# Performance work log

Measured on AMD Instinct MI355X. Metric: run time of the kernel, lower is better.

## Reference

```python
import jax, jax.numpy as jnp
import numpy as np

N_NODES = 50000
D_FEAT = 128
N_EDGES = 1_600_000
NUM_ITERATIONS = 20  # init kwarg num_iterations


def setup_inputs() -> dict:
    key = jax.random.key(0)
    k1, k2, k3 = jax.random.split(key, 3)
    x = jax.random.normal(k1, (N_NODES, D_FEAT), dtype=jnp.float32)
    edge_index = jax.random.randint(k2, (2, N_EDGES), 0, N_NODES, dtype=jnp.int32)
    mask = jax.random.bernoulli(k3, 0.5, (N_NODES, D_FEAT))  # True where feature is known
    return {"x": x, "edge_index": edge_index, "mask": mask}


def reference(x, edge_index, mask):
    row, col = edge_index[0], edge_index[1]
    # D^-1/2 A D^-1/2 edge weights (degree computed over col, as in the torch code)
    deg = jax.ops.segment_sum(jnp.ones((N_EDGES,), x.dtype), col, num_segments=N_NODES)
    deg_inv_sqrt = jnp.where(deg > 0, jax.lax.rsqrt(deg), 0.0)
    w = deg_inv_sqrt[row] * deg_inv_sqrt[col]  # [n_edges]

    out0 = jnp.where(mask, x, 0.0)  # zero out unknown features

    def body(_, out):
        # SpMM: result[i] = sum over edges e with row[e]==i of w[e] * out[col[e]]
        msg = w[:, None] * out[col]  # [n_edges, d]
        out = jax.ops.segment_sum(msg, row, num_segments=N_NODES)
        return jnp.where(mask, x, out)  # reset known features each iteration

    return jax.lax.fori_loop(0, NUM_ITERATIONS, body, out0)
```

## Files before the change

kernel.cpp:

```cpp
#include <hip/hip_runtime.h>

#define N_NODES 50000
#define D_FEAT 128
#define N_EDGES 1600000
#define NUM_ITERS 20
#define ZERO_NODE N_NODES
#define HNB 128
#define HALF_NODES 25000
#define NB 196
#define BCAP 192
#define ABLK 128
#define PAD 4
#define STAGE_CAP 12544
#define CSR_MAX (N_EDGES + PAD * N_NODES)

typedef unsigned int u32;
typedef unsigned short u16;
typedef unsigned long long u64;

__device__ __forceinline__ u16 bf16_rne(float f) {
    u32 u = __float_as_uint(f);
    u32 r = u + 0x7fffu + ((u >> 16) & 1u);
    return (u16)(r >> 16);
}

__global__ void detect_kernel(const u32* __restrict__ w, int nwords,
                              u32* __restrict__ flags) {
    int i = blockIdx.x * blockDim.x + threadIdx.x;
    int stride = gridDim.x * blockDim.x;
    u32 f = 0;
    for (; i < nwords; i += stride) {
        u32 v = w[i];
        if (v > 1u) f |= 1u;
        if (v == 0x3f800000u) f |= 2u;
    }
    if (f) atomicOr(flags, f);
}

__global__ void __launch_bounds__(256) hist_kernel(const int* __restrict__ idx,
                                                   u32* __restrict__ partial, int n) {
    __shared__ u32 h[HALF_NODES / 2];
    for (int i = threadIdx.x; i < HALF_NODES / 2; i += 256) h[i] = 0;
    __syncthreads();
    const int half = blockIdx.x >> 7;
    const int bid = blockIdx.x & (HNB - 1);
    const int base_node = half * HALF_NODES;
    int i = bid * 256 + threadIdx.x;
    const int stride = HNB * 256;
    for (; i < n; i += stride) {
        u32 r = (u32)(idx[i] - base_node);
        if (r < (u32)HALF_NODES) atomicAdd(&h[r >> 1], 1u << ((r & 1) * 16));
    }
    __syncthreads();
    u32* dst = partial + (size_t)bid * (N_NODES / 2) + half * (HALF_NODES / 2);
    for (int j = threadIdx.x; j < HALF_NODES / 2; j += 256) dst[j] = h[j];
}

__global__ void reduce_dis_kernel(const u32* __restrict__ pA, float* __restrict__ dis) {
    int i = blockIdx.x * blockDim.x + threadIdx.x;
    if (i >= N_NODES / 2) return;
    u32 sa = 0;
    for (int b = 0; b < HNB; ++b) sa += pA[(size_t)b * (N_NODES / 2) + i];
    int d0 = (int)(sa & 0xffffu), d1 = (int)(sa >> 16);
    dis[2 * i]     = d0 ? rsqrtf((float)d0) : 0.0f;
    dis[2 * i + 1] = d1 ? rsqrtf((float)d1) : 0.0f;
}

__global__ void __launch_bounds__(256) bucketA_kernel(const int* __restrict__ row,
                                                      const int* __restrict__ col,
                                                      u32* __restrict__ bucket,
                                                      int* __restrict__ bcnt) {
    __shared__ u32 cur[NB];
    for (int i = threadIdx.x; i < NB; i += 256) cur[i] = 0;
    __syncthreads();
    u32* myreg = bucket + (size_t)blockIdx.x * NB * BCAP;
    int i = blockIdx.x * 256 + threadIdx.x;
    int stride = gridDim.x * 256;
    for (; i < N_EDGES; i += stride) {
        int r = row[i];
        int b = r >> 8;
        u32 pos = atomicAdd(&cur[b], 1u);
        if (pos < (u32)BCAP)
            myreg[(size_t)b * BCAP + pos] = ((u32)(r & 255) << 16) | (u32)col[i];
    }
    __syncthreads();
    for (int i2 = threadIdx.x; i2 < NB; i2 += 256)
        bcnt[blockIdx.x * NB + i2] = (int)min(cur[i2], (u32)BCAP);
}

__global__ void __launch_bounds__(256) b1_kernel(const u32* __restrict__ bucket,
                                                 const int* __restrict__ bcnt,
                                                 int* __restrict__ cnt_p) {
    const int b = blockIdx.x;
    const int tid = threadIdx.x;
    __shared__ int pfx[ABLK + 1];
    __shared__ int cnts[ABLK];
    __shared__ u32 hist[256];
    if (tid < 256) hist[tid] = 0;
    if (tid < ABLK) cnts[tid] = bcnt[tid * NB + b];
    __syncthreads();
    if (tid == 0) {
        int s = 0;
        for (int k = 0; k < ABLK; ++k) { pfx[k] = s; s += cnts[k]; }
        pfx[ABLK] = s;
    }
    __syncthreads();
    const int total = pfx[ABLK];
    for (int t = tid; t < total; t += 256) {
        int lo = 0, hi = ABLK;
        while (hi - lo > 1) { int mid = (lo + hi) >> 1; if (pfx[mid] <= t) lo = mid; else hi = mid; }
        u32 e = bucket[(size_t)lo * NB * BCAP + (size_t)b * BCAP + (t - pfx[lo])];
        atomicAdd(&hist[e >> 16], 1u);
    }
    __syncthreads();
    const int r0 = b << 8;
    if (tid < 256) {
        int r = r0 + tid;
        if (r < N_NODES) cnt_p[r] = ((int)hist[tid] + (PAD - 1)) & ~(PAD - 1);
    }
}

__global__ void __launch_bounds__(1024) scan_kernel(const int* __restrict__ cnt,
                                                    int* __restrict__ offsets, int n) {
    __shared__ int wsum[16];
    __shared__ int s_carry;
    const int tid = threadIdx.x;
    const int lane = tid & 63, wid = tid >> 6;
    if (tid == 0) s_carry = 0;
    __syncthreads();
    for (int base = 0; base < n; base += 4096) {
        int i4 = base + tid * 4;
        int4 v = make_int4(0, 0, 0, 0);
        if (i4 < n) v = *(const int4*)(cnt + i4);
        int e1 = v.x, e2 = v.x + v.y, e3 = e2 + v.z, tot = e3 + v.w;
        int winc = tot;
        #pragma unroll
        for (int off = 1; off < 64; off <<= 1) {
            int t = __shfl_up(winc, off);
            if (lane >= off) winc += t;
        }
        if (lane == 63) wsum[wid] = winc;
        __syncthreads();
        if (tid < 16) {
            int s = wsum[tid];
            #pragma unroll
            for (int off = 1; off < 16; off <<= 1) {
                int t = __shfl_up(s, off);
                if (tid >= off) s += t;
            }
            wsum[tid] = s;
        }
        __syncthreads();
        int bb = s_carry + (wid ? wsum[wid - 1] : 0) + winc - tot;
        if (i4 < n) *(int4*)(offsets + i4) = make_int4(bb, bb + e1, bb + e2, bb + e3);
        __syncthreads();
        if (tid == 0) s_carry += wsum[15];
        __syncthreads();
    }
    if (tid == 0) offsets[n] = s_carry;
}

__global__ void __launch_bounds__(256) b2_kernel(const u32* __restrict__ bucket,
                                                 const int* __restrict__ bcnt,
                                                 const int* __restrict__ offsets,
                                                 u16* __restrict__ csr) {
    const int b = blockIdx.x;
    const int tid = threadIdx.x;
    const int r0 = b << 8;
    const int rcount = min(256, N_NODES - r0);
    __shared__ int pfx[ABLK + 1];
    __shared__ int cnts[ABLK];
    __shared__ int lbase[257];
    __shared__ u32 lcur[256];
    __shared__ __align__(16) u16 stage[STAGE_CAP];
    if (tid < ABLK) cnts[tid] = bcnt[tid * NB + b];
    for (int j = tid; j <= rcount; j += 256) lbase[j] = offsets[r0 + j] - offsets[r0];
    if (tid < 256) lcur[tid] = 0;
    __syncthreads();
    if (tid == 0) {
        int s = 0;
        for (int k = 0; k < ABLK; ++k) { pfx[k] = s; s += cnts[k]; }
        pfx[ABLK] = s;
    }
    __syncthreads();
    const int total = pfx[ABLK];
    const int L = min(lbase[rcount], STAGE_CAP);
    for (int j = tid; j < L; j += 256) stage[j] = (u16)ZERO_NODE;
    __syncthreads();
    for (int t = tid; t < total; t += 256) {
        int lo = 0, hi = ABLK;
        while (hi - lo > 1) { int mid = (lo + hi) >> 1; if (pfx[mid] <= t) lo = mid; else hi = mid; }
        u32 e = bucket[(size_t)lo * NB * BCAP + (size_t)b * BCAP + (t - pfx[lo])];
        int lr = (int)(e >> 16);
        u32 p = atomicAdd(&lcur[lr], 1u);
        int idx = lbase[lr] + (int)p;
        if (idx < STAGE_CAP) stage[idx] = (u16)(e & 0xffffu);
    }
    __syncthreads();
    uint4* dst = (uint4*)(csr + offsets[r0]);
    const uint4* src = (const uint4*)stage;
    for (int j = tid; j < (L >> 3); j += 256) dst[j] = src[j];
    if (tid == 0 && (L & 7)) {
        uint2* d2 = (uint2*)(csr + offsets[r0] + (L & ~7));
        const uint2* s2 = (const uint2*)(stage + (L & ~7));
        *d2 = *s2;
    }
}

__global__ void build_kernel(const void* __restrict__ mask,
                             const u32* __restrict__ flags,
                             const float* __restrict__ x,
                             const float* __restrict__ dis,
                             u32* __restrict__ bits,
                             u16* __restrict__ sxm, int n) {
    int i = blockIdx.x * blockDim.x + threadIdx.x;
    if (i >= n) return;
    u32 fl = *flags;
    int mv;
    if ((fl & 1u) == 0u) {
        mv = ((const int*)mask)[i];
    } else if (fl & 2u) {
        mv = (((const float*)mask)[i] != 0.0f) ? 1 : 0;
    } else {
        mv = ((const unsigned char*)mask)[i];
    }
    bool pred = (mv != 0);
    u64 b = __ballot(pred);
    int lane = threadIdx.x & 63;
    if (lane == 0)  bits[i >> 5] = (u32)b;
    if (lane == 32) bits[i >> 5] = (u32)(b >> 32);
    sxm[i] = pred ? bf16_rne(dis[i >> 7] * x[i]) : (u16)0;
}

template <bool FINAL>
__global__ void __launch_bounds__(256) prop_kernel(const int* __restrict__ offsets,
                                                   const u16* __restrict__ csr,
                                                   const u16* __restrict__ cur,
                                                   const u32* __restrict__ bits,
                                                   const float* __restrict__ dis,
                                                   const u16* __restrict__ sxm,
                                                   const float* __restrict__ x,
                                                   void* __restrict__ nxtp) {
    const int tid = threadIdx.x;
    const int wid = tid >> 6, lane = tid & 63;
    const int node = blockIdx.x * 4 + wid;
    if (node >= N_NODES) return;
    const int fl = lane & 15, eg = lane >> 4;
    const int s = offsets[node], e = offsets[node + 1];

    float a0 = 0, a1 = 0, a2 = 0, a3 = 0, a4 = 0, a5 = 0, a6 = 0, a7 = 0;
    #pragma unroll 8
    for (int base = s; base < e; base += 4) {
        const int c = (int)csr[base + eg];
        const uint4 r = *((const uint4*)(cur + (size_t)c * D_FEAT) + fl);
        a0 += __uint_as_float(r.x << 16);
        a1 += __uint_as_float(r.x & 0xffff0000u);
        a2 += __uint_as_float(r.y << 16);
        a3 += __uint_as_float(r.y & 0xffff0000u);
        a4 += __uint_as_float(r.z << 16);
        a5 += __uint_as_float(r.z & 0xffff0000u);
        a6 += __uint_as_float(r.w << 16);
        a7 += __uint_as_float(r.w & 0xffff0000u);
    }
    a0 += __shfl_xor(a0, 16); a0 += __shfl_xor(a0, 32);
    a1 += __shfl_xor(a1, 16); a1 += __shfl_xor(a1, 32);
    a2 += __shfl_xor(a2, 16); a2 += __shfl_xor(a2, 32);
    a3 += __shfl_xor(a3, 16); a3 += __shfl_xor(a3, 32);
    a4 += __shfl_xor(a4, 16); a4 += __shfl_xor(a4, 32);
    a5 += __shfl_xor(a5, 16); a5 += __shfl_xor(a5, 32);
    a6 += __shfl_xor(a6, 16); a6 += __shfl_xor(a6, 32);
    a7 += __shfl_xor(a7, 16); a7 += __shfl_xor(a7, 32);

    if (eg == 0) {
        const int fbase = node * D_FEAT + fl * 8;
        const u32 mb = (bits[node * 4 + (fl >> 2)] >> ((fl & 3) * 8)) & 0xffu;
        const float dr = dis[node];
        if (FINAL) {
            const float4 x0 = *(const float4*)(x + fbase);
            const float4 x1 = *(const float4*)(x + fbase + 4);
            float* outp = (float*)nxtp;
            float4 o0, o1;
            o0.x = (mb & 0x01u) ? x0.x : dr * a0;
            o0.y = (mb & 0x02u) ? x0.y : dr * a1;
            o0.z = (mb & 0x04u) ? x0.z : dr * a2;
            o0.w = (mb & 0x08u) ? x0.w : dr * a3;
            o1.x = (mb & 0x10u) ? x1.x : dr * a4;
            o1.y = (mb & 0x20u) ? x1.y : dr * a5;
            o1.z = (mb & 0x40u) ? x1.z : dr * a6;
            o1.w = (mb & 0x80u) ? x1.w : dr * a7;
            *(float4*)(outp + fbase) = o0;
            *(float4*)(outp + fbase + 4) = o1;
        } else {
            const float d2 = dr * dr;
            const uint4 sv = *(const uint4*)(sxm + fbase);
            u16 t0 = (mb & 0x01u) ? (u16)(sv.x)       : bf16_rne(d2 * a0);
            u16 t1 = (mb & 0x02u) ? (u16)(sv.x >> 16) : bf16_rne(d2 * a1);
            u16 t2 = (mb & 0x04u) ? (u16)(sv.y)       : bf16_rne(d2 * a2);
            u16 t3 = (mb & 0x08u) ? (u16)(sv.y >> 16) : bf16_rne(d2 * a3);
            u16 t4 = (mb & 0x10u) ? (u16)(sv.z)       : bf16_rne(d2 * a4);
            u16 t5 = (mb & 0x20u) ? (u16)(sv.z >> 16) : bf16_rne(d2 * a5);
            u16 t6 = (mb & 0x40u) ? (u16)(sv.w)       : bf16_rne(d2 * a6);
            u16 t7 = (mb & 0x80u) ? (u16)(sv.w >> 16) : bf16_rne(d2 * a7);
            uint4 st;
            st.x = (u32)t0 | ((u32)t1 << 16);
            st.y = (u32)t2 | ((u32)t3 << 16);
            st.z = (u32)t4 | ((u32)t5 << 16);
            st.w = (u32)t6 | ((u32)t7 << 16);
            *(uint4*)(((u16*)nxtp) + fbase) = st;
        }
    }
}

extern "C" void kernel_launch(void* const* d_in, const int* in_sizes, int n_in,
                              void* d_out, int out_size, void* d_ws, size_t ws_size,
                              hipStream_t stream) {
    const float* x = (const float*)d_in[0];
    const int* edge = (const int*)d_in[1];
    const void* mask = d_in[2];
    const int* row = edge;
    const int* col = edge + N_EDGES;
    float* out = (float*)d_out;

    char* ws = (char*)d_ws;
    size_t off = 0;
    auto alloc = [&](size_t bytes) -> void* {
        void* p = ws + off;
        off += (bytes + 255) & ~(size_t)255;
        return p;
    };
    const size_t state_elems = (size_t)(N_NODES + 1) * D_FEAT;
    int*   offsets = (int*)alloc((size_t)(N_NODES + 1) * 4);
    int*   cnt_p   = (int*)alloc((size_t)N_NODES * 4);
    float* dis     = (float*)alloc((size_t)N_NODES * 4);
    u32*   flags   = (u32*)alloc(256);
    u32*   bits    = (u32*)alloc((size_t)N_NODES * D_FEAT / 8);
    u32*   pA      = (u32*)alloc((size_t)HNB * (N_NODES / 2) * 4);
    u32*   bucket  = (u32*)alloc((size_t)ABLK * NB * BCAP * 4);
    int*   bcnt    = (int*)alloc((size_t)ABLK * NB * 4);
    u16*   csr     = (u16*)alloc((size_t)CSR_MAX * 2);
    u16*   sxm     = (u16*)alloc(state_elems * 2);
    u16*   stA     = (u16*)alloc(state_elems * 2);
    u16*   stB     = (u16*)alloc(state_elems * 2);

    hipMemsetAsync(flags, 0, 4, stream);
    hipMemsetAsync(sxm + (size_t)N_NODES * D_FEAT, 0, D_FEAT * 2, stream);
    hipMemsetAsync(stA + (size_t)N_NODES * D_FEAT, 0, D_FEAT * 2, stream);
    hipMemsetAsync(stB + (size_t)N_NODES * D_FEAT, 0, D_FEAT * 2, stream);

    const int total_feat = N_NODES * D_FEAT;
    const int mask_words = total_feat / 4;

    detect_kernel<<<1024, 256, 0, stream>>>((const u32*)mask, mask_words, flags);
    hist_kernel<<<2 * HNB, 256, 0, stream>>>(col, pA, N_EDGES);
    reduce_dis_kernel<<<(N_NODES / 2 + 255) / 256, 256, 0, stream>>>(pA, dis);
    bucketA_kernel<<<ABLK, 256, 0, stream>>>(row, col, bucket, bcnt);
    b1_kernel<<<NB, 256, 0, stream>>>(bucket, bcnt, cnt_p);
    scan_kernel<<<1, 1024, 0, stream>>>(cnt_p, offsets, N_NODES);
    build_kernel<<<total_feat / 256, 256, 0, stream>>>(mask, flags, x, dis, bits, sxm, total_feat);
    b2_kernel<<<NB, 256, 0, stream>>>(bucket, bcnt, offsets, csr);

    const int prop_blocks = (N_NODES + 3) / 4;
    const u16* src = sxm;
    for (int it = 0; it < NUM_ITERS; ++it) {
        if (it < NUM_ITERS - 1) {
            u16* dst = (it & 1) ? stB : stA;
            prop_kernel<false><<<prop_blocks, 256, 0, stream>>>(offsets, csr, src, bits, dis, sxm, x, dst);
            src = dst;
        } else {
            prop_kernel<true><<<prop_blocks, 256, 0, stream>>>(offsets, csr, src, bits, dis, sxm, x, out);
        }
    }
}
```

Baseline: 1.146 ms.

## Slice feature state into 16-wide column panels and stage CSR chunks in LDS

```diff
diff --git a/kernel.cpp b/kernel.cpp
--- a/kernel.cpp
+++ b/kernel.cpp
@@ -14,9 +14,16 @@
 #define STAGE_CAP 12544
 #define CSR_MAX (N_EDGES + PAD * N_NODES)
 
+#define SLICES 8
+#define SFEAT 16
+#define NPB 32
+#define CSR_LDS_CAP 4096
+
 typedef unsigned int u32;
 typedef unsigned short u16;
 typedef unsigned long long u64;
+
+#define SLICE_ELEMS ((size_t)(N_NODES + 1) * SFEAT)
 
 __device__ __forceinline__ u16 bf16_rne(float f) {
     u32 u = __float_as_uint(f);
@@ -211,8 +218,9 @@
                              const u32* __restrict__ flags,
                              const float* __restrict__ x,
                              const float* __restrict__ dis,
-                             u32* __restrict__ bits,
-                             u16* __restrict__ sxm, int n) {
+                             u32* __restrict__ bits_s,
+                             u16* __restrict__ sxm_s,
+                             int n) {
     int i = blockIdx.x * blockDim.x + threadIdx.x;
     if (i >= n) return;
     u32 fl = *flags;
@@ -227,32 +235,69 @@
     bool pred = (mv != 0);
     u64 b = __ballot(pred);
     int lane = threadIdx.x & 63;
-    if (lane == 0)  bits[i >> 5] = (u32)b;
-    if (lane == 32) bits[i >> 5] = (u32)(b >> 32);
-    sxm[i] = pred ? bf16_rne(dis[i >> 7] * x[i]) : (u16)0;
+    int wIdx = i >> 5;
+    if (lane == 0)  bits_s[(size_t)(wIdx & 3) * N_NODES + (wIdx >> 2)] = (u32)b;
+    if (lane == 32) bits_s[(size_t)(wIdx & 3) * N_NODES + (wIdx >> 2)] = (u32)(b >> 32);
+    const int node = i >> 7, f = i & 127;
+    const int sl = f >> 4, wi = f & 15;
+    sxm_s[(size_t)sl * SLICE_ELEMS + (size_t)node * SFEAT + wi] =
+        pred ? bf16_rne(dis[node] * x[i]) : (u16)0;
+}
+
+__global__ void zero_rows_kernel(u16* __restrict__ a, u16* __restrict__ b,
+                                 u16* __restrict__ c) {
+    int t = threadIdx.x;
+    if (t < SLICES * SFEAT) {
+        int s = t >> 4, e = t & 15;
+        size_t g = (size_t)s * SLICE_ELEMS + (size_t)N_NODES * SFEAT + e;
+        a[g] = 0; b[g] = 0; c[g] = 0;
+    }
 }
 
 template <bool FINAL>
 __global__ void __launch_bounds__(256) prop_kernel(const int* __restrict__ offsets,
                                                    const u16* __restrict__ csr,
                                                    const u16* __restrict__ cur,
-                                                   const u32* __restrict__ bits,
+                                                   const u32* __restrict__ bits_s,
                                                    const float* __restrict__ dis,
-                                                   const u16* __restrict__ sxm,
+                                                   const u16* __restrict__ sxm_s,
                                                    const float* __restrict__ x,
                                                    void* __restrict__ nxtp) {
+    const int bid = blockIdx.x;
+    const int slice = bid & (SLICES - 1);
+    const int chunk = bid >> 3;
+    const int n0 = chunk * NPB;
     const int tid = threadIdx.x;
+
+    __shared__ int soff[NPB + 1];
+    __shared__ __align__(8) u16 csr_lds[CSR_LDS_CAP];
+
+    if (tid <= NPB) soff[tid] = offsets[min(n0 + tid, N_NODES)];
+    __syncthreads();
+    const int s0 = soff[0];
+    const int span = min(soff[NPB] - s0, CSR_LDS_CAP);
+    {
+        const uint2* gsrc = (const uint2*)(csr + s0);
+        uint2* ldst = (uint2*)csr_lds;
+        for (int j = tid; j * 4 < span; j += 256) ldst[j] = gsrc[j];
+    }
+    __syncthreads();
+
     const int wid = tid >> 6, lane = tid & 63;
-    const int node = blockIdx.x * 4 + wid;
-    if (node >= N_NODES) return;
-    const int fl = lane & 15, eg = lane >> 4;
-    const int s = offsets[node], e = offsets[node + 1];
+    const int nd = lane >> 3;
+    const int fl = (lane >> 2) & 1;
+    const int eg = lane & 3;
+    const int node = n0 + wid * 8 + nd;
+
+    const u16* curs = cur + (size_t)slice * SLICE_ELEMS;
+    const int li = wid * 8 + nd;
+    const int sl = soff[li] - s0, el = soff[li + 1] - s0;
 
     float a0 = 0, a1 = 0, a2 = 0, a3 = 0, a4 = 0, a5 = 0, a6 = 0, a7 = 0;
-    #pragma unroll 8
-    for (int base = s; base < e; base += 4) {
-        const int c = (int)csr[base + eg];
-        const uint4 r = *((const uint4*)(cur + (size_t)c * D_FEAT) + fl);
+    #pragma unroll 4
+    for (int b = sl; b < el; b += 4) {
+        const int c = (int)csr_lds[b + eg];
+        const uint4 r = *((const uint4*)(curs + (size_t)c * SFEAT) + fl);
         a0 += __uint_as_float(r.x << 16);
         a1 += __uint_as_float(r.x & 0xffff0000u);
         a2 += __uint_as_float(r.y << 16);
@@ -262,22 +307,23 @@
         a6 += __uint_as_float(r.w << 16);
         a7 += __uint_as_float(r.w & 0xffff0000u);
     }
-    a0 += __shfl_xor(a0, 16); a0 += __shfl_xor(a0, 32);
-    a1 += __shfl_xor(a1, 16); a1 += __shfl_xor(a1, 32);
-    a2 += __shfl_xor(a2, 16); a2 += __shfl_xor(a2, 32);
-    a3 += __shfl_xor(a3, 16); a3 += __shfl_xor(a3, 32);
-    a4 += __shfl_xor(a4, 16); a4 += __shfl_xor(a4, 32);
-    a5 += __shfl_xor(a5, 16); a5 += __shfl_xor(a5, 32);
-    a6 += __shfl_xor(a6, 16); a6 += __shfl_xor(a6, 32);
-    a7 += __shfl_xor(a7, 16); a7 += __shfl_xor(a7, 32);
-
-    if (eg == 0) {
-        const int fbase = node * D_FEAT + fl * 8;
-        const u32 mb = (bits[node * 4 + (fl >> 2)] >> ((fl & 3) * 8)) & 0xffu;
+    a0 += __shfl_xor(a0, 1); a0 += __shfl_xor(a0, 2);
+    a1 += __shfl_xor(a1, 1); a1 += __shfl_xor(a1, 2);
+    a2 += __shfl_xor(a2, 1); a2 += __shfl_xor(a2, 2);
+    a3 += __shfl_xor(a3, 1); a3 += __shfl_xor(a3, 2);
+    a4 += __shfl_xor(a4, 1); a4 += __shfl_xor(a4, 2);
+    a5 += __shfl_xor(a5, 1); a5 += __shfl_xor(a5, 2);
+    a6 += __shfl_xor(a6, 1); a6 += __shfl_xor(a6, 2);
+    a7 += __shfl_xor(a7, 1); a7 += __shfl_xor(a7, 2);
+
+    if (eg == 0 && node < N_NODES) {
+        const u32 w = bits_s[(size_t)(slice >> 1) * N_NODES + node];
+        const u32 mb = (w >> (((slice & 1) << 4) + (fl << 3))) & 0xffu;
         const float dr = dis[node];
         if (FINAL) {
-            const float4 x0 = *(const float4*)(x + fbase);
-            const float4 x1 = *(const float4*)(x + fbase + 4);
+            const int fb = node * D_FEAT + slice * SFEAT + fl * 8;
+            const float4 x0 = *(const float4*)(x + fb);
+            const float4 x1 = *(const float4*)(x + fb + 4);
             float* outp = (float*)nxtp;
             float4 o0, o1;
             o0.x = (mb & 0x01u) ? x0.x : dr * a0;
@@ -288,11 +334,12 @@
             o1.y = (mb & 0x20u) ? x1.y : dr * a5;
             o1.z = (mb & 0x40u) ? x1.z : dr * a6;
             o1.w = (mb & 0x80u) ? x1.w : dr * a7;
-            *(float4*)(outp + fbase) = o0;
-            *(float4*)(outp + fbase + 4) = o1;
+            *(float4*)(outp + fb) = o0;
+            *(float4*)(outp + fb + 4) = o1;
         } else {
             const float d2 = dr * dr;
-            const uint4 sv = *(const uint4*)(sxm + fbase);
+            const size_t g = (size_t)slice * SLICE_ELEMS + (size_t)node * SFEAT + fl * 8;
+            const uint4 sv = *(const uint4*)(sxm_s + g);
             u16 t0 = (mb & 0x01u) ? (u16)(sv.x)       : bf16_rne(d2 * a0);
             u16 t1 = (mb & 0x02u) ? (u16)(sv.x >> 16) : bf16_rne(d2 * a1);
             u16 t2 = (mb & 0x04u) ? (u16)(sv.y)       : bf16_rne(d2 * a2);
@@ -306,7 +353,7 @@
             st.y = (u32)t2 | ((u32)t3 << 16);
             st.z = (u32)t4 | ((u32)t5 << 16);
             st.w = (u32)t6 | ((u32)t7 << 16);
-            *(uint4*)(((u16*)nxtp) + fbase) = st;
+            *(uint4*)(((u16*)nxtp) + g) = st;
         }
     }
 }
@@ -328,24 +375,20 @@
         off += (bytes + 255) & ~(size_t)255;
         return p;
     };
-    const size_t state_elems = (size_t)(N_NODES + 1) * D_FEAT;
     int*   offsets = (int*)alloc((size_t)(N_NODES + 1) * 4);
     int*   cnt_p   = (int*)alloc((size_t)N_NODES * 4);
     float* dis     = (float*)alloc((size_t)N_NODES * 4);
     u32*   flags   = (u32*)alloc(256);
-    u32*   bits    = (u32*)alloc((size_t)N_NODES * D_FEAT / 8);
+    u32*   bits_s  = (u32*)alloc((size_t)4 * N_NODES * 4);
     u32*   pA      = (u32*)alloc((size_t)HNB * (N_NODES / 2) * 4);
     u32*   bucket  = (u32*)alloc((size_t)ABLK * NB * BCAP * 4);
     int*   bcnt    = (int*)alloc((size_t)ABLK * NB * 4);
     u16*   csr     = (u16*)alloc((size_t)CSR_MAX * 2);
-    u16*   sxm     = (u16*)alloc(state_elems * 2);
-    u16*   stA     = (u16*)alloc(state_elems * 2);
-    u16*   stB     = (u16*)alloc(state_elems * 2);
+    u16*   sxm_s   = (u16*)alloc((size_t)SLICES * SLICE_ELEMS * 2);
+    u16*   stA     = (u16*)alloc((size_t)SLICES * SLICE_ELEMS * 2);
+    u16*   stB     = (u16*)alloc((size_t)SLICES * SLICE_ELEMS * 2);
 
     hipMemsetAsync(flags, 0, 4, stream);
-    hipMemsetAsync(sxm + (size_t)N_NODES * D_FEAT, 0, D_FEAT * 2, stream);
-    hipMemsetAsync(stA + (size_t)N_NODES * D_FEAT, 0, D_FEAT * 2, stream);
-    hipMemsetAsync(stB + (size_t)N_NODES * D_FEAT, 0, D_FEAT * 2, stream);
 
     const int total_feat = N_NODES * D_FEAT;
     const int mask_words = total_feat / 4;
@@ -356,18 +399,20 @@
     bucketA_kernel<<<ABLK, 256, 0, stream>>>(row, col, bucket, bcnt);
     b1_kernel<<<NB, 256, 0, stream>>>(bucket, bcnt, cnt_p);
     scan_kernel<<<1, 1024, 0, stream>>>(cnt_p, offsets, N_NODES);
-    build_kernel<<<total_feat / 256, 256, 0, stream>>>(mask, flags, x, dis, bits, sxm, total_feat);
+    build_kernel<<<total_feat / 256, 256, 0, stream>>>(mask, flags, x, dis, bits_s, sxm_s, total_feat);
     b2_kernel<<<NB, 256, 0, stream>>>(bucket, bcnt, offsets, csr);
-
-    const int prop_blocks = (N_NODES + 3) / 4;
-    const u16* src = sxm;
+    zero_rows_kernel<<<1, 256, 0, stream>>>(sxm_s, stA, stB);
+
+    const int chunks = (N_NODES + NPB - 1) / NPB;
+    const int prop_blocks = SLICES * chunks;
+    const u16* src = sxm_s;
     for (int it = 0; it < NUM_ITERS; ++it) {
         if (it < NUM_ITERS - 1) {
             u16* dst = (it & 1) ? stB : stA;
-            prop_kernel<false><<<prop_blocks, 256, 0, stream>>>(offsets, csr, src, bits, dis, sxm, x, dst);
+            prop_kernel<false><<<prop_blocks, 256, 0, stream>>>(offsets, csr, src, bits_s, dis, sxm_s, x, dst);
             src = dst;
         } else {
-            prop_kernel<true><<<prop_blocks, 256, 0, stream>>>(offsets, csr, src, bits, dis, sxm, x, out);
+            prop_kernel<true><<<prop_blocks, 256, 0, stream>>>(offsets, csr, src, bits_s, dis, sxm_s, x, out);
         }
     }
 }
```

After: 1.343 ms. +17.1%, slower.
